# Kernel tuning notes

Hardware: AMD Instinct MI355X
Metric: run time of the kernel (lower is better)

Reference implementation:

```python
import jax, jax.numpy as jnp
import numpy as np
from jax import lax

EPS = 1e-6

def _ln(x):
    # LayerNorm32 over channel dim, computed in fp32
    x32 = x.astype(jnp.float32)
    mu = jnp.mean(x32, axis=-1, keepdims=True)
    var = jnp.mean(jnp.square(x32 - mu), axis=-1, keepdims=True)
    return ((x32 - mu) * lax.rsqrt(var + EPS)).astype(x.dtype)

def _downsample2(f, mask):
    # mean over active voxels in each 2x2x2 cell; f must already be zero at inactive voxels
    B, D, H, W, C = f.shape
    fs = f.reshape(B, D // 2, 2, H // 2, 2, W // 2, 2, C).sum(axis=(2, 4, 6))
    cnt = mask.reshape(B, D // 2, 2, H // 2, 2, W // 2, 2).astype(f.dtype).sum(axis=(2, 4, 6))
    out = fs / jnp.maximum(cnt, 1.0)[..., None]
    return out, cnt > 0

def _subm_conv3(x, w, b, mask_f):
    # submanifold sparse conv == dense SAME conv on zero-filled grid, masked to active set
    y = lax.conv_general_dilated(x, w, window_strides=(1, 1, 1), padding='SAME',
                                 dimension_numbers=('NDHWC', 'DHWIO', 'NDHWC'))
    return (y + b) * mask_f


def setup_inputs() -> dict:
    key = jax.random.key(0)
    ks = jax.random.split(key, 6)
    B, D, C, CO = 4, 64, 64, 128
    feats = jax.random.normal(ks[0], (B, D, D, D, C), jnp.float32)
    mask = jax.random.uniform(ks[1], (B, D, D, D)) < 0.3
    gamma1 = jnp.ones((C,), jnp.float32)
    beta1 = jnp.zeros((C,), jnp.float32)
    w1 = jax.random.normal(ks[2], (3, 3, 3, C, CO), jnp.float32) / np.sqrt(27.0 * C)
    b1 = jnp.zeros((CO,), jnp.float32)
    # conv2 is zero-initialized in the original (zero_module); we use small random
    # weights so the reference is numerically non-degenerate
    w2 = jax.random.normal(ks[3], (3, 3, 3, CO, CO), jnp.float32) / np.sqrt(27.0 * CO)
    b2 = jnp.zeros((CO,), jnp.float32)
    w_skip = jax.random.normal(ks[4], (C, CO), jnp.float32) / np.sqrt(C)
    b_skip = jnp.zeros((CO,), jnp.float32)
    return dict(feats=feats, mask=mask, gamma1=gamma1, beta1=beta1,
                w1=w1, b1=b1, w2=w2, b2=b2, w_skip=w_skip, b_skip=b_skip)


def reference(feats, mask, gamma1, beta1, w1, b1, w2, b2, w_skip, b_skip):
    m = mask[..., None].astype(feats.dtype)          # [B,D,H,W,1]
    h = (_ln(feats) * gamma1 + beta1)                # norm1 (affine)
    h = jax.nn.silu(h) * m                           # silu, restrict to active set
    xm = feats * m
    h, mask2 = _downsample2(h, mask)                 # SparseDownsample(2) on h
    x_ds, _ = _downsample2(xm, mask)                 # SparseDownsample(2) on x
    m2 = mask2[..., None].astype(feats.dtype)
    h = _subm_conv3(h, w1, b1, m2)                   # conv1
    h = jax.nn.silu(_ln(h)) * m2                     # norm2 (no affine) + silu
    h = _subm_conv3(h, w2, b2, m2)                   # conv2
    skip = (x_ds @ w_skip + b_skip) * m2             # SparseLinear skip
    return h + skip
```

## Files before the change

kernel.cpp:

```cpp
#include <hip/hip_runtime.h>
#include <hip/hip_bf16.h>

#define EPS 1e-6f
typedef unsigned short b16;
typedef __attribute__((ext_vector_type(8))) short v8s;
typedef __attribute__((ext_vector_type(4))) float v4f;

typedef const __attribute__((address_space(1))) void* gptr_t;
typedef __attribute__((address_space(3))) void* lptr_t;

__device__ __forceinline__ b16 f2b(float f) {
    __hip_bfloat16 h = __float2bfloat16(f);
    return *reinterpret_cast<b16*>(&h);
}
__device__ __forceinline__ float siluf(float x){ return x / (1.f + __expf(-x)); }

__device__ __forceinline__ void gll16(const b16* g, b16* l) {
    __builtin_amdgcn_global_load_lds((gptr_t)g, (lptr_t)l, 16, 0, 0);
}

template<int IC>
__global__ void __launch_bounds__(256) k_wt(const float* __restrict__ w, b16* __restrict__ o, int tot) {
    int i = blockIdx.x*256 + threadIdx.x;
    if (i >= tot) return;
    int ic = i % IC; int oc = (i / IC) & 127; int tap = i / (IC*128);
    o[i] = f2b(w[(tap*IC + ic)*128 + oc]);
}

template<int IC>
__global__ void __launch_bounds__(256) k_wtb(const float* __restrict__ w, b16* __restrict__ o, int tot) {
    int i = blockIdx.x*256 + threadIdx.x;
    if (i >= tot) return;
    constexpr int ICB = IC/32;
    int icl = i & 31;
    int oc  = (i >> 5) & 127;
    int r   = i >> 12;
    int tap = r / ICB, icb = r % ICB;
    o[i] = f2b(w[(tap*IC + icb*32 + icl)*128 + oc]);
}

__global__ void __launch_bounds__(256) k_ln_down(
    const float* __restrict__ feats, const int* __restrict__ mask,
    const float* __restrict__ gamma, const float* __restrict__ beta,
    b16* __restrict__ h_ds_pad, b16* __restrict__ x_ds, float* __restrict__ cnt_out)
{
    int wave = (blockIdx.x * 256 + threadIdx.x) >> 6;
    int lane = threadIdx.x & 63;
    int x = wave & 31, y = (wave >> 5) & 31, z = (wave >> 10) & 31, b = wave >> 15;
    float g = gamma[lane], be = beta[lane];
    float hacc = 0.f, xacc = 0.f, cnt = 0.f;
    #pragma unroll
    for (int i = 0; i < 8; ++i) {
        int zz = 2*z + (i>>2), yy = 2*y + ((i>>1)&1), xx = 2*x + (i&1);
        int vox = ((b*64 + zz)*64 + yy)*64 + xx;
        int m = mask[vox];
        float val = feats[vox*64 + lane];
        float s1 = val, s2 = val*val;
        #pragma unroll
        for (int off = 32; off > 0; off >>= 1) {
            s1 += __shfl_xor(s1, off, 64);
            s2 += __shfl_xor(s2, off, 64);
        }
        float mu = s1 * (1.f/64.f);
        float var = fmaxf(s2 * (1.f/64.f) - mu*mu, 0.f);
        float h = (val - mu) * rsqrtf(var + EPS) * g + be;
        h = siluf(h);
        if (m != 0) { hacc += h; xacc += val; cnt += 1.f; }
    }
    float inv = 1.f / fmaxf(cnt, 1.f);
    long vp = ((long)(b*34 + z+1)*34 + (y+1))*34 + (x+1);
    h_ds_pad[vp*64 + lane] = f2b(hacc * inv);
    x_ds[(long)wave*64 + lane] = f2b(xacc * inv);
    if (lane == 0) cnt_out[wave] = cnt;
}

template<int IC, bool IS_CONV1>
__global__ void __launch_bounds__(256) k_conv_mfma(
    const b16* __restrict__ inp,
    const b16* __restrict__ wt,
    const float* __restrict__ bias,
    const float* __restrict__ cnt,
    const b16* __restrict__ x_ds,
    const b16* __restrict__ wst,
    const float* __restrict__ b_skip,
    b16* __restrict__ h2out,
    float* __restrict__ out)
{
    constexpr int ICB = IC/32;
    constexpr int NK = 27*ICB;
    __shared__ b16 lA[2][4096];
    __shared__ b16 lB[2][4096];

    int bid = blockIdx.x;
    int y0 = (bid & 7) << 2;
    int z  = (bid >> 3) & 31;
    int b  = bid >> 8;
    int t  = threadIdx.x;
    int lane = t & 63;
    int w = t >> 6;
    int col = lane & 15;
    int quad = lane >> 4;

    const b16* gAsrc[2];
    const b16* gBsrc[2];
    {
        int vsub = lane >> 2;
        int s    = lane & 3;
        #pragma unroll
        for (int j = 0; j < 2; ++j) {
            int x  = j*16 + vsub;
            int cA = (s - (x >> 1)) & 3;
            gAsrc[j] = inp + ((long)((b*34 + z)*34 + (y0 + w))*34 + x)*IC + cA*8;
            int oc = w*32 + j*16 + vsub;
            int cB = (s - (vsub >> 1)) & 3;
            gBsrc[j] = wt + oc*32 + cB*8;
        }
    }

    int so   = ((quad + (col>>1)) & 3) * 8;
    int aoff = w*1024 + col*32 + so;
    int boff = col*32 + so;

    v4f acc[2][8];
    #pragma unroll
    for (int tl=0;tl<2;++tl)
        #pragma unroll
        for (int n=0;n<8;++n) acc[tl][n] = (v4f){0.f,0.f,0.f,0.f};

    long offAn = 0;
    int icbn = 0, kxn = 0, kyn = 0;
    auto advance = [&]() {
        ++icbn; offAn += 32;
        if (icbn == ICB) {
            icbn = 0;
            ++kxn;
            if (kxn == 3) {
                kxn = 0; ++kyn;
                if (kyn == 3) { kyn = 0; offAn += (long)(34*34 - 2*34 - 3)*IC; }
                else          {           offAn += (long)(34 - 3)*IC; }
            }
        }
    };

    auto stage = [&](long offA, long offB, int buf) {
        #pragma unroll
        for (int j = 0; j < 2; ++j) {
            gll16(gAsrc[j] + offA, &lA[buf][w*1024 + j*512]);
            gll16(gBsrc[j] + offB, &lB[buf][w*1024 + j*512]);
        }
    };

    stage(0, 0, 0);
    advance();
    long offBn = 4096;
    __syncthreads();

    int cur = 0;
    for (int k = 0; k < NK; ++k) {
        if (k + 1 < NK) {
            stage(offAn, offBn, cur ^ 1);
            advance();
            offBn += 4096;
        }
        v8s a0 = *(const v8s*)(&lA[cur][aoff]);
        v8s a1 = *(const v8s*)(&lA[cur][aoff + 512]);
        __builtin_amdgcn_s_setprio(1);
        #pragma unroll
        for (int n = 0; n < 8; ++n) {
            v8s bb = *(const v8s*)(&lB[cur][n*512 + boff]);
            acc[0][n] = __builtin_amdgcn_mfma_f32_16x16x32_bf16(a0, bb, acc[0][n], 0,0,0);
            acc[1][n] = __builtin_amdgcn_mfma_f32_16x16x32_bf16(a1, bb, acc[1][n], 0,0,0);
        }
        __builtin_amdgcn_s_setprio(0);
        __syncthreads();
        cur ^= 1;
    }

    int yrow = y0 + w;
    long cellrow = ((long)(b*32+z)*32 + yrow)*32;

    if (!IS_CONV1) {
        const b16* X0 = x_ds + (cellrow + col)*64 + quad*8;
        const b16* X1 = X0 + 16*64;
        const b16* WS = wst + col*64 + quad*8;
        #pragma unroll
        for (int s = 0; s < 2; ++s) {
            v8s a0 = *(const v8s*)(X0 + s*32);
            v8s a1 = *(const v8s*)(X1 + s*32);
            #pragma unroll
            for (int n=0;n<8;++n) {
                v8s bb = *(const v8s*)(WS + n*16*64 + s*32);
                acc[0][n] = __builtin_amdgcn_mfma_f32_16x16x32_bf16(a0, bb, acc[0][n], 0,0,0);
                acc[1][n] = __builtin_amdgcn_mfma_f32_16x16x32_bf16(a1, bb, acc[1][n], 0,0,0);
            }
        }
    }

    float bv[8];
    #pragma unroll
    for (int n=0;n<8;++n)
        bv[n] = bias[n*16+col] + (IS_CONV1 ? 0.f : b_skip[n*16+col]);

    long prow = ((long)(b*34 + z+1)*34 + (yrow+1))*34 + 1;

    #pragma unroll
    for (int tl=0; tl<2; ++tl) {
        if (IS_CONV1) {
            float s1[4], s2[4];
            #pragma unroll
            for (int r=0;r<4;++r){
                float a=0.f, q=0.f;
                #pragma unroll
                for (int n=0;n<8;++n){ float v = acc[tl][n][r] + bv[n]; a+=v; q+=v*v; }
                s1[r]=a; s2[r]=q;
            }
            #pragma unroll
            for (int off=1; off<16; off<<=1){
                #pragma unroll
                for (int r=0;r<4;++r){ s1[r]+=__shfl_xor(s1[r],off); s2[r]+=__shfl_xor(s2[r],off); }
            }
            #pragma unroll
            for (int r=0;r<4;++r){
                int row = quad*4 + r;
                int x = tl*16 + row;
                float c = cnt[cellrow + x];
                float mu = s1[r]*(1.f/128.f);
                float var = fmaxf(s2[r]*(1.f/128.f) - mu*mu, 0.f);
                float rs = rsqrtf(var + EPS);
                bool act = c > 0.f;
                #pragma unroll
                for (int n=0;n<8;++n){
                    float v = acc[tl][n][r] + bv[n];
                    float hv = act ? siluf((v-mu)*rs) : 0.f;
                    h2out[(prow + x)*128 + n*16 + col] = f2b(hv);
                }
            }
        } else {
            #pragma unroll
            for (int r=0;r<4;++r){
                int row = quad*4 + r;
                int x = tl*16 + row;
                float c = cnt[cellrow + x];
                bool act = c > 0.f;
                #pragma unroll
                for (int n=0;n<8;++n){
                    float v = acc[tl][n][r] + bv[n];
                    out[(cellrow + x)*128 + n*16 + col] = act ? v : 0.f;
                }
            }
        }
    }
}

extern "C" void kernel_launch(void* const* d_in, const int* in_sizes, int n_in,
                              void* d_out, int out_size, void* d_ws, size_t ws_size,
                              hipStream_t stream) {
    const float* feats  = (const float*)d_in[0];
    const int*   mask   = (const int*)  d_in[1];
    const float* gamma1 = (const float*)d_in[2];
    const float* beta1  = (const float*)d_in[3];
    const float* w1     = (const float*)d_in[4];
    const float* b1     = (const float*)d_in[5];
    const float* w2     = (const float*)d_in[6];
    const float* b2     = (const float*)d_in[7];
    const float* w_skip = (const float*)d_in[8];
    const float* b_skip = (const float*)d_in[9];
    float* out = (float*)d_out;

    char* ws = (char*)d_ws;
    b16*   h_ds_pad = (b16*)(ws);
    b16*   h2_pad   = (b16*)(ws + 20123648);
    b16*   x_ds     = (b16*)(ws + 60370944);
    float* cnt      = (float*)(ws + 77148160);
    b16*   w1t      = (b16*)(ws + 77672448);
    b16*   w2t      = (b16*)(ws + 78114816);
    b16*   wst      = (b16*)(ws + 78999552);

    hipMemsetAsync(h_ds_pad, 0, 20123648, stream);
    hipMemsetAsync(h2_pad,   0, 40247296, stream);

    const int n_w1 = 27*64*128;
    const int n_w2 = 27*128*128;
    const int n_ws = 64*128;
    k_wtb<64> <<<(n_w1 + 255)/256, 256, 0, stream>>>(w1, w1t, n_w1);
    k_wtb<128><<<(n_w2 + 255)/256, 256, 0, stream>>>(w2, w2t, n_w2);
    k_wt<64>  <<<(n_ws + 255)/256, 256, 0, stream>>>(w_skip, wst, n_ws);

    k_ln_down<<<32768, 256, 0, stream>>>(feats, mask, gamma1, beta1, h_ds_pad, x_ds, cnt);

    k_conv_mfma<64,true><<<1024, 256, 0, stream>>>(h_ds_pad, w1t, b1, cnt,
                                                   nullptr, nullptr, nullptr,
                                                   h2_pad, nullptr);
    k_conv_mfma<128,false><<<1024, 256, 0, stream>>>(h2_pad, w2t, b2, cnt,
                                                     x_ds, wst, b_skip,
                                                     nullptr, out);
}
```

Measured before the change: 734.0 us.

## Replace LDS-staged conv operand loads with direct global-to-register double buffering

The conv kernels no longer stage A and B tiles through shared memory with global_load_lds and per-step barriers. Each lane now loads its MFMA operands straight from global memory into registers, using two register sets as a ping-pong buffer. This removes the LDS traffic and the __syncthreads per K step. In exchange, the four waves each fetch the same weights separately with no shared reuse, and more registers are held live, which may cut occupancy.

```diff
diff --git a/kernel.cpp b/kernel.cpp
--- a/kernel.cpp
+++ b/kernel.cpp
@@ -6,18 +6,11 @@
 typedef __attribute__((ext_vector_type(8))) short v8s;
 typedef __attribute__((ext_vector_type(4))) float v4f;
 
-typedef const __attribute__((address_space(1))) void* gptr_t;
-typedef __attribute__((address_space(3))) void* lptr_t;
-
 __device__ __forceinline__ b16 f2b(float f) {
     __hip_bfloat16 h = __float2bfloat16(f);
     return *reinterpret_cast<b16*>(&h);
 }
 __device__ __forceinline__ float siluf(float x){ return x / (1.f + __expf(-x)); }
-
-__device__ __forceinline__ void gll16(const b16* g, b16* l) {
-    __builtin_amdgcn_global_load_lds((gptr_t)g, (lptr_t)l, 16, 0, 0);
-}
 
 template<int IC>
 __global__ void __launch_bounds__(256) k_wt(const float* __restrict__ w, b16* __restrict__ o, int tot) {
@@ -75,7 +68,7 @@
 }
 
 template<int IC, bool IS_CONV1>
-__global__ void __launch_bounds__(256) k_conv_mfma(
+__device__ __forceinline__ void conv_body(
     const b16* __restrict__ inp,
     const b16* __restrict__ wt,
     const float* __restrict__ bias,
@@ -88,8 +81,6 @@
 {
     constexpr int ICB = IC/32;
     constexpr int NK = 27*ICB;
-    __shared__ b16 lA[2][4096];
-    __shared__ b16 lB[2][4096];
 
     int bid = blockIdx.x;
     int y0 = (bid & 7) << 2;
@@ -101,25 +92,8 @@
     int col = lane & 15;
     int quad = lane >> 4;
 
-    const b16* gAsrc[2];
-    const b16* gBsrc[2];
-    {
-        int vsub = lane >> 2;
-        int s    = lane & 3;
-        #pragma unroll
-        for (int j = 0; j < 2; ++j) {
-            int x  = j*16 + vsub;
-            int cA = (s - (x >> 1)) & 3;
-            gAsrc[j] = inp + ((long)((b*34 + z)*34 + (y0 + w))*34 + x)*IC + cA*8;
-            int oc = w*32 + j*16 + vsub;
-            int cB = (s - (vsub >> 1)) & 3;
-            gBsrc[j] = wt + oc*32 + cB*8;
-        }
-    }
-
-    int so   = ((quad + (col>>1)) & 3) * 8;
-    int aoff = w*1024 + col*32 + so;
-    int boff = col*32 + so;
+    const b16* gA = inp + ((long)((b*34 + z)*34 + (y0 + w))*34 + col)*IC + quad*8;
+    const b16* gB = wt + col*32 + quad*8;
 
     v4f acc[2][8];
     #pragma unroll
@@ -127,53 +101,55 @@
         #pragma unroll
         for (int n=0;n<8;++n) acc[tl][n] = (v4f){0.f,0.f,0.f,0.f};
 
-    long offAn = 0;
+    long offA = 0;
     int icbn = 0, kxn = 0, kyn = 0;
     auto advance = [&]() {
-        ++icbn; offAn += 32;
+        ++icbn; offA += 32;
         if (icbn == ICB) {
             icbn = 0;
             ++kxn;
             if (kxn == 3) {
                 kxn = 0; ++kyn;
-                if (kyn == 3) { kyn = 0; offAn += (long)(34*34 - 2*34 - 3)*IC; }
-                else          {           offAn += (long)(34 - 3)*IC; }
-            }
-        }
-    };
-
-    auto stage = [&](long offA, long offB, int buf) {
-        #pragma unroll
-        for (int j = 0; j < 2; ++j) {
-            gll16(gAsrc[j] + offA, &lA[buf][w*1024 + j*512]);
-            gll16(gBsrc[j] + offB, &lB[buf][w*1024 + j*512]);
-        }
-    };
-
-    stage(0, 0, 0);
+                if (kyn == 3) { kyn = 0; offA += (long)(34*34 - 2*34 - 3)*IC; }
+                else          {           offA += (long)(34 - 3)*IC; }
+            }
+        }
+    };
+
+    auto loadA = [&](long oA, v8s& A0, v8s& A1) {
+        A0 = *(const v8s*)(gA + oA);
+        A1 = *(const v8s*)(gA + oA + 16*IC);
+    };
+    auto loadB = [&](long oB, v8s (&BB)[8]) {
+        #pragma unroll
+        for (int n = 0; n < 8; ++n) BB[n] = *(const v8s*)(gB + oB + n*512);
+    };
+    auto mfma_step = [&](const v8s& A0, const v8s& A1, const v8s (&BB)[8]) {
+        #pragma unroll
+        for (int n = 0; n < 8; ++n) {
+            acc[0][n] = __builtin_amdgcn_mfma_f32_16x16x32_bf16(A0, BB[n], acc[0][n], 0,0,0);
+            acc[1][n] = __builtin_amdgcn_mfma_f32_16x16x32_bf16(A1, BB[n], acc[1][n], 0,0,0);
+        }
+    };
+
+    v8s a0A, a1A, a0B, a1B;
+    v8s bbA[8], bbB[8];
+
+    loadA(0, a0A, a1A);
+    loadB(0, bbA);
     advance();
-    long offBn = 4096;
-    __syncthreads();
-
-    int cur = 0;
-    for (int k = 0; k < NK; ++k) {
-        if (k + 1 < NK) {
-            stage(offAn, offBn, cur ^ 1);
+
+    for (int k = 0; k < NK; k += 2) {
+        loadA(offA, a0B, a1B);
+        loadB((long)(k+1) << 12, bbB);
+        advance();
+        mfma_step(a0A, a1A, bbA);
+        if (k + 2 < NK) {
+            loadA(offA, a0A, a1A);
+            loadB((long)(k+2) << 12, bbA);
             advance();
-            offBn += 4096;
-        }
-        v8s a0 = *(const v8s*)(&lA[cur][aoff]);
-        v8s a1 = *(const v8s*)(&lA[cur][aoff + 512]);
-        __builtin_amdgcn_s_setprio(1);
-        #pragma unroll
-        for (int n = 0; n < 8; ++n) {
-            v8s bb = *(const v8s*)(&lB[cur][n*512 + boff]);
-            acc[0][n] = __builtin_amdgcn_mfma_f32_16x16x32_bf16(a0, bb, acc[0][n], 0,0,0);
-            acc[1][n] = __builtin_amdgcn_mfma_f32_16x16x32_bf16(a1, bb, acc[1][n], 0,0,0);
-        }
-        __builtin_amdgcn_s_setprio(0);
-        __syncthreads();
-        cur ^= 1;
+        }
+        mfma_step(a0B, a1B, bbB);
     }
 
     int yrow = y0 + w;
@@ -250,6 +226,23 @@
             }
         }
     }
+}
+
+__global__ void __launch_bounds__(256) k_conv1(
+    const b16* __restrict__ inp, const b16* __restrict__ wt,
+    const float* __restrict__ bias, const float* __restrict__ cnt,
+    b16* __restrict__ h2out)
+{
+    conv_body<64, true>(inp, wt, bias, cnt, nullptr, nullptr, nullptr, h2out, nullptr);
+}
+
+__global__ void __launch_bounds__(256) k_conv2(
+    const b16* __restrict__ inp, const b16* __restrict__ wt,
+    const float* __restrict__ bias, const float* __restrict__ cnt,
+    const b16* __restrict__ x_ds, const b16* __restrict__ wst,
+    const float* __restrict__ b_skip, float* __restrict__ out)
+{
+    conv_body<128, false>(inp, wt, bias, cnt, x_ds, wst, b_skip, nullptr, out);
 }
 
 extern "C" void kernel_launch(void* const* d_in, const int* in_sizes, int n_in,
@@ -288,10 +281,6 @@
 
     k_ln_down<<<32768, 256, 0, stream>>>(feats, mask, gamma1, beta1, h_ds_pad, x_ds, cnt);
 
-    k_conv_mfma<64,true><<<1024, 256, 0, stream>>>(h_ds_pad, w1t, b1, cnt,
-                                                   nullptr, nullptr, nullptr,
-                                                   h2_pad, nullptr);
-    k_conv_mfma<128,false><<<1024, 256, 0, stream>>>(h2_pad, w2t, b2, cnt,
-                                                     x_ds, wst, b_skip,
-                                                     nullptr, out);
-}
+    k_conv1<<<1024, 256, 0, stream>>>(h_ds_pad, w1t, b1, cnt, h2_pad);
+    k_conv2<<<1024, 256, 0, stream>>>(h2_pad, w2t, b2, cnt, x_ds, wst, b_skip, out);
+}
```

After: 894.9 us. 1.22x slower.
